# Optimization experiments

Measured on AMD Instinct MI355X. Metric: run time of the kernel, lower is better.

Reference implementation:

```python
import jax, jax.numpy as jnp
import numpy as np

NUM_NODES = 50000
NUM_EDGES = 800000
NUM_FEATURES = 128
HIDDEN = 128
NUM_CLASSES = 40


def setup_inputs() -> dict:
    key = jax.random.key(0)
    ks = jax.random.split(key, 10)
    x = jax.random.normal(ks[0], (NUM_NODES, NUM_FEATURES), dtype=jnp.float32)
    edge_index = jax.random.randint(ks[1], (2, NUM_EDGES), 0, NUM_NODES, dtype=jnp.int32)
    def glorot(k, fan_in, fan_out):
        s = jnp.sqrt(6.0 / (fan_in + fan_out))
        return jax.random.uniform(k, (fan_in, fan_out), jnp.float32, -s, s)
    return {
        "x": x,
        "edge_index": edge_index,
        "W1": glorot(ks[2], NUM_FEATURES, HIDDEN), "b1": jnp.zeros((HIDDEN,), jnp.float32),
        "W2": glorot(ks[3], HIDDEN, HIDDEN),       "b2": jnp.zeros((HIDDEN,), jnp.float32),
        "W3": glorot(ks[4], HIDDEN, HIDDEN),       "b3": jnp.zeros((HIDDEN,), jnp.float32),
        "Wc": glorot(ks[5], HIDDEN, NUM_CLASSES),  "bc": jnp.zeros((NUM_CLASSES,), jnp.float32),
    }


def _gcn_norm(edge_index, num_nodes, dtype):
    # add self-loops, symmetric normalization D^{-1/2} (A+I) D^{-1/2}
    loops = jnp.arange(num_nodes, dtype=edge_index.dtype)
    src = jnp.concatenate([edge_index[0], loops])
    dst = jnp.concatenate([edge_index[1], loops])
    deg = jax.ops.segment_sum(jnp.ones_like(dst, dtype=dtype), dst, num_segments=num_nodes)
    dinv = jnp.where(deg > 0, jax.lax.rsqrt(deg), 0.0)
    norm = dinv[src] * dinv[dst]  # [E + N]
    return src, dst, norm


def _gcn_conv(h, W, b, src, dst, norm, num_nodes):
    h = h @ W                                  # [N, out]
    msg = h[src] * norm[:, None]               # gather + scale  [E+N, out]
    agg = jax.ops.segment_sum(msg, dst, num_segments=num_nodes)
    return agg + b


def reference(x, edge_index, W1, b1, W2, b2, W3, b3, Wc, bc):
    N = x.shape[0]
    src, dst, norm = _gcn_norm(edge_index, N, x.dtype)
    h = jax.nn.relu(_gcn_conv(x, W1, b1, src, dst, norm, N))
    h = jax.nn.relu(_gcn_conv(h, W2, b2, src, dst, norm, N))
    h = jax.nn.relu(_gcn_conv(h, W3, b3, src, dst, norm, N))
    out = h @ Wc + bc
    return (out, h)
```

## Files before the change

kernel.cpp:

```cpp
#include <hip/hip_runtime.h>

typedef float f32x4 __attribute__((ext_vector_type(4)));
typedef short s16x8 __attribute__((ext_vector_type(8)));

__device__ __forceinline__ float us2f(unsigned short u) {
    union { unsigned int i; float f; } v;
    v.i = ((unsigned int)u) << 16;
    return v.f;
}
__device__ __forceinline__ unsigned short f2us(float f) {
    union { unsigned int i; float f; } v; v.f = f;
    unsigned int r = v.i + 0x7fff + ((v.i >> 16) & 1);
    return (unsigned short)(r >> 16);
}

__global__ void k_wprep(const float* __restrict__ W1, const float* __restrict__ W2,
                        const float* __restrict__ W3, const float* __restrict__ Wc,
                        unsigned short* __restrict__ img, int* __restrict__ bcnt) {
    int b = blockIdx.x >> 7;
    int n = threadIdx.x;
    if (b >= 4) { bcnt[n] = 0; bcnt[n + 128] = 0; return; }
    int k = blockIdx.x & 127;
    unsigned short *H, *L;
    float f;
    if (b < 3) {
        const float* W = (b == 0) ? W1 : ((b == 1) ? W2 : W3);
        H = img + b * 32768; L = H + 16384;
        f = W[k * 128 + n];
    } else {
        if (n >= 48) return;
        H = img + 3 * 32768; L = H + 6144;
        f = (n < 40) ? Wc[k * 40 + n] : 0.f;
    }
    unsigned short h = f2us(f);
    unsigned short l = f2us(f - us2f(h));
    int idx = n * 128 + ((((k >> 3) ^ (n & 15))) << 3) + (k & 7);
    H[idx] = h; L[idx] = l;
}

__global__ __launch_bounds__(256) void k_hist(const int* __restrict__ dst, int E, int chunk,
                                              int* __restrict__ bcnt) {
    __shared__ int cnt[256];
    int t = threadIdx.x;
    cnt[t] = 0; __syncthreads();
    int s = blockIdx.x * chunk;
    int e = s + chunk; if (e > E) e = E;
    for (int i = s + t; i < e; i += 256) atomicAdd(&cnt[dst[i] >> 8], 1);
    __syncthreads();
    if (cnt[t]) atomicAdd(&bcnt[t], cnt[t]);
}

__global__ void k_bscan(const int* __restrict__ bcnt, int* __restrict__ bofs,
                        int* __restrict__ gcur) {
    __shared__ int s[256];
    int t = threadIdx.x;
    int v = bcnt[t];
    s[t] = v; __syncthreads();
    for (int off = 1; off < 256; off <<= 1) {
        int x = (t >= off) ? s[t - off] : 0;
        __syncthreads();
        s[t] += x;
        __syncthreads();
    }
    int ex = s[t] - v;
    bofs[t] = ex; gcur[t] = ex;
    if (t == 255) bofs[256] = s[255];
}

__global__ __launch_bounds__(256) void k_scatter1(const int* __restrict__ src,
                                                  const int* __restrict__ dst, int E, int chunk,
                                                  int* __restrict__ gcur,
                                                  unsigned int* __restrict__ pk) {
    __shared__ int cnt[256];
    int t = threadIdx.x;
    cnt[t] = 0; __syncthreads();
    int s = blockIdx.x * chunk;
    int e = s + chunk; if (e > E) e = E;
    for (int i = s + t; i < e; i += 256) atomicAdd(&cnt[dst[i] >> 8], 1);
    __syncthreads();
    int base = atomicAdd(&gcur[t], cnt[t]);
    cnt[t] = base;
    __syncthreads();
    for (int i = s + t; i < e; i += 256) {
        int d = dst[i];
        int slot = atomicAdd(&cnt[d >> 8], 1);
        pk[slot] = ((unsigned int)src[i] << 8) | (unsigned int)(d & 255);
    }
}

__global__ __launch_bounds__(256) void k_degscan(const unsigned int* __restrict__ pk,
                                                 const int* __restrict__ bofs,
                                                 int* __restrict__ row_ptr,
                                                 int* __restrict__ bsum,
                                                 float* __restrict__ dinv, int N) {
    __shared__ int cnt[256];
    __shared__ int s[256];
    int t = threadIdx.x, b = blockIdx.x;
    cnt[t] = 0; __syncthreads();
    int s0 = bofs[b], s1 = bofs[b + 1];
    for (int i = s0 + t; i < s1; i += 256) atomicAdd(&cnt[pk[i] & 255], 1);
    __syncthreads();
    int v = cnt[t];
    s[t] = v; __syncthreads();
    for (int off = 1; off < 256; off <<= 1) {
        int x = (t >= off) ? s[t - off] : 0;
        __syncthreads();
        s[t] += x;
        __syncthreads();
    }
    int node = (b << 8) + t;
    if (node < N) {
        row_ptr[node] = s[t] - v;
        dinv[node] = rsqrtf((float)(v + 1));
    }
    if (t == 255) bsum[b] = s[255];
}

__global__ void k_scan2(int* __restrict__ bsum, int nb) {
    __shared__ int s[256];
    int t = threadIdx.x;
    int v = (t < nb) ? bsum[t] : 0;
    s[t] = v; __syncthreads();
    for (int off = 1; off < 256; off <<= 1) {
        int x = (t >= off) ? s[t - off] : 0;
        __syncthreads();
        s[t] += x;
        __syncthreads();
    }
    if (t < nb) bsum[t] = s[t] - v;
}

__global__ __launch_bounds__(256) void k_scatter2(const unsigned int* __restrict__ pk,
                                                  const int* __restrict__ bofs,
                                                  int* __restrict__ row_ptr,
                                                  const int* __restrict__ bsum,
                                                  int* __restrict__ csr, int N, int E) {
    __shared__ int cur[256];
    int t = threadIdx.x, b = blockIdx.x;
    int node = (b << 8) + t;
    int rp = 0;
    if (node < N) {
        rp = row_ptr[node] + bsum[b];
        row_ptr[node] = rp;
    }
    cur[t] = rp;
    __syncthreads();
    int s = bofs[b], e = bofs[b + 1];
    for (int i = s + t; i < e; i += 256) {
        unsigned int v = pk[i];
        int slot = atomicAdd(&cur[v & 255], 1);
        csr[slot] = (int)(v >> 8);
    }
    if (node == N - 1) row_ptr[N] = E;
}

__global__ __launch_bounds__(256) void k_gemm128m(const float* __restrict__ A,
                                                  const unsigned short* __restrict__ img,
                                                  const float* __restrict__ dinv,
                                                  unsigned short* __restrict__ M, int N) {
    __shared__ __align__(16) unsigned short WsH[16384];
    __shared__ __align__(16) unsigned short WsL[16384];
    int t = threadIdx.x;
    {
        const uint4* s = (const uint4*)img;
        uint4* dH = (uint4*)WsH; uint4* dL = (uint4*)WsL;
#pragma unroll
        for (int i = 0; i < 8; i++) dH[t + i * 256] = s[t + i * 256];
#pragma unroll
        for (int i = 0; i < 8; i++) dL[t + i * 256] = s[2048 + t + i * 256];
    }
    __syncthreads();

    int w = t >> 6, lane = t & 63;
    int m = lane & 15, q = lane >> 4;
    int row0 = blockIdx.x * 64 + w * 16;
    int gr = row0 + m;
    int grc = (gr < N) ? gr : (N - 1);
    const float4* Arow = (const float4*)(A + (size_t)grc * 128);
    int nbase = m * 128;

    f32x4 acc[8];
#pragma unroll
    for (int cb = 0; cb < 8; cb++) { acc[cb][0]=0.f; acc[cb][1]=0.f; acc[cb][2]=0.f; acc[cb][3]=0.f; }

#pragma unroll
    for (int ks = 0; ks < 4; ks++) {
        float4 f0 = Arow[ks * 8 + q * 2];
        float4 f1 = Arow[ks * 8 + q * 2 + 1];
        float fv[8] = {f0.x, f0.y, f0.z, f0.w, f1.x, f1.y, f1.z, f1.w};
        union { unsigned short u[8]; s16x8 v; } ah, al;
#pragma unroll
        for (int j = 0; j < 8; j++) {
            unsigned short h = f2us(fv[j]);
            ah.u[j] = h;
            al.u[j] = f2us(fv[j] - us2f(h));
        }
        int koff = (((ks * 4 + q) ^ m) & 15) << 3;
#pragma unroll
        for (int cb = 0; cb < 8; cb++) {
            int o = cb * 2048 + nbase + koff;
            s16x8 wh = *(const s16x8*)&WsH[o];
            s16x8 wl = *(const s16x8*)&WsL[o];
            acc[cb] = __builtin_amdgcn_mfma_f32_16x16x32_bf16(ah.v, wh, acc[cb], 0, 0, 0);
            acc[cb] = __builtin_amdgcn_mfma_f32_16x16x32_bf16(ah.v, wl, acc[cb], 0, 0, 0);
            acc[cb] = __builtin_amdgcn_mfma_f32_16x16x32_bf16(al.v, wh, acc[cb], 0, 0, 0);
        }
    }

#pragma unroll
    for (int r = 0; r < 4; r++) {
        int grow = row0 + q * 4 + r;
        if (grow < N) {
            float dv = dinv[grow];
#pragma unroll
            for (int cb = 0; cb < 8; cb++)
                M[(size_t)grow * 128 + cb * 16 + m] = f2us(acc[cb][r] * dv);
        }
    }
}

__global__ __launch_bounds__(256) void k_gemm40m(const float* __restrict__ A,
                                                 const unsigned short* __restrict__ img,
                                                 const float* __restrict__ bc,
                                                 float* __restrict__ out, int N) {
    __shared__ __align__(16) unsigned short WsH[6144];
    __shared__ __align__(16) unsigned short WsL[6144];
    int t = threadIdx.x;
    {
        const uint4* s = (const uint4*)img;
        uint4* dH = (uint4*)WsH; uint4* dL = (uint4*)WsL;
#pragma unroll
        for (int i = 0; i < 3; i++) dH[t + i * 256] = s[t + i * 256];
#pragma unroll
        for (int i = 0; i < 3; i++) dL[t + i * 256] = s[768 + t + i * 256];
    }
    __syncthreads();

    int w = t >> 6, lane = t & 63;
    int m = lane & 15, q = lane >> 4;
    int row0 = blockIdx.x * 64 + w * 16;
    int gr = row0 + m;
    int grc = (gr < N) ? gr : (N - 1);
    const float4* Arow = (const float4*)(A + (size_t)grc * 128);
    int nbase = m * 128;

    f32x4 acc[3];
#pragma unroll
    for (int cb = 0; cb < 3; cb++) { acc[cb][0]=0.f; acc[cb][1]=0.f; acc[cb][2]=0.f; acc[cb][3]=0.f; }

#pragma unroll
    for (int ks = 0; ks < 4; ks++) {
        float4 f0 = Arow[ks * 8 + q * 2];
        float4 f1 = Arow[ks * 8 + q * 2 + 1];
        float fv[8] = {f0.x, f0.y, f0.z, f0.w, f1.x, f1.y, f1.z, f1.w};
        union { unsigned short u[8]; s16x8 v; } ah, al;
#pragma unroll
        for (int j = 0; j < 8; j++) {
            unsigned short h = f2us(fv[j]);
            ah.u[j] = h;
            al.u[j] = f2us(fv[j] - us2f(h));
        }
        int koff = (((ks * 4 + q) ^ m) & 15) << 3;
#pragma unroll
        for (int cb = 0; cb < 3; cb++) {
            int o = cb * 2048 + nbase + koff;
            s16x8 wh = *(const s16x8*)&WsH[o];
            s16x8 wl = *(const s16x8*)&WsL[o];
            acc[cb] = __builtin_amdgcn_mfma_f32_16x16x32_bf16(ah.v, wh, acc[cb], 0, 0, 0);
            acc[cb] = __builtin_amdgcn_mfma_f32_16x16x32_bf16(ah.v, wl, acc[cb], 0, 0, 0);
            acc[cb] = __builtin_amdgcn_mfma_f32_16x16x32_bf16(al.v, wh, acc[cb], 0, 0, 0);
        }
    }

#pragma unroll
    for (int r = 0; r < 4; r++) {
        int grow = row0 + q * 4 + r;
        if (grow < N) {
#pragma unroll
            for (int cb = 0; cb < 3; cb++) {
                int col = cb * 16 + m;
                if (col < 40) out[(size_t)grow * 40 + col] = acc[cb][r] + bc[col];
            }
        }
    }
}

__global__ __launch_bounds__(256) void k_gather(const unsigned short* __restrict__ M,
                                                const int* __restrict__ csr,
                                                const int* __restrict__ row_ptr,
                                                const float* __restrict__ dinv,
                                                const float* __restrict__ bias,
                                                float* __restrict__ H, int N) {
    int w    = (blockIdx.x << 2) + (threadIdx.x >> 6);
    int lane = threadIdx.x & 63;
    if (w >= N) return;
    int g  = lane >> 4;
    int sl = lane & 15;

    const uint4* M16 = (const uint4*)M;
    float acc[8];
#pragma unroll
    for (int i = 0; i < 8; i++) acc[i] = 0.f;

    auto accum = [&](uint4 tv) {
        unsigned int uu[4] = {tv.x, tv.y, tv.z, tv.w};
#pragma unroll
        for (int i = 0; i < 4; i++) {
            acc[2 * i]     += us2f((unsigned short)(uu[i] & 0xffffu));
            acc[2 * i + 1] += us2f((unsigned short)(uu[i] >> 16));
        }
    };

    if (g == 0) accum(M16[(size_t)w * 16 + sl]);

    int s0 = row_ptr[w], s1 = row_ptr[w + 1];
    for (int base = s0; base < s1; base += 64) {
        int n = s1 - base; if (n > 64) n = 64;
        int idx = (lane < n) ? csr[base + lane] : 0;
        int full = n >> 2;
        int rem  = n & 3;
        int j = 0;
        for (; j + 4 <= full; j += 4) {
            int u0 = __shfl(idx, (j + 0) * 4 + g);
            int u1 = __shfl(idx, (j + 1) * 4 + g);
            int u2 = __shfl(idx, (j + 2) * 4 + g);
            int u3 = __shfl(idx, (j + 3) * 4 + g);
            uint4 t0 = M16[(size_t)u0 * 16 + sl];
            uint4 t1 = M16[(size_t)u1 * 16 + sl];
            uint4 t2 = M16[(size_t)u2 * 16 + sl];
            uint4 t3 = M16[(size_t)u3 * 16 + sl];
            accum(t0); accum(t1); accum(t2); accum(t3);
        }
        for (; j < full; j++) {
            int u = __shfl(idx, j * 4 + g);
            accum(M16[(size_t)u * 16 + sl]);
        }
        int ur = __shfl(idx, ((full << 2) + g) & 63);
        if (g < rem) accum(M16[(size_t)ur * 16 + sl]);
    }

#pragma unroll
    for (int i = 0; i < 8; i++) {
        acc[i] += __shfl_xor(acc[i], 16);
        acc[i] += __shfl_xor(acc[i], 32);
    }

    float dv = dinv[w];
    const float4* b4 = (const float4*)bias;
    float4 b0 = b4[sl * 2], b1 = b4[sl * 2 + 1];
    float4 o0, o1;
    o0.x = fmaxf(fmaf(dv, acc[0], b0.x), 0.f);
    o0.y = fmaxf(fmaf(dv, acc[1], b0.y), 0.f);
    o0.z = fmaxf(fmaf(dv, acc[2], b0.z), 0.f);
    o0.w = fmaxf(fmaf(dv, acc[3], b0.w), 0.f);
    o1.x = fmaxf(fmaf(dv, acc[4], b1.x), 0.f);
    o1.y = fmaxf(fmaf(dv, acc[5], b1.y), 0.f);
    o1.z = fmaxf(fmaf(dv, acc[6], b1.z), 0.f);
    o1.w = fmaxf(fmaf(dv, acc[7], b1.w), 0.f);

    if (g == 0) {
        float4* H4 = (float4*)H;
        H4[(size_t)w * 32 + sl * 2]     = o0;
        H4[(size_t)w * 32 + sl * 2 + 1] = o1;
    }
}

extern "C" void kernel_launch(void* const* d_in, const int* in_sizes, int n_in,
                              void* d_out, int out_size, void* d_ws, size_t ws_size,
                              hipStream_t stream) {
    const float* x  = (const float*)d_in[0];
    const int*   ei = (const int*)d_in[1];
    const float* W1 = (const float*)d_in[2];
    const float* b1 = (const float*)d_in[3];
    const float* W2 = (const float*)d_in[4];
    const float* b2 = (const float*)d_in[5];
    const float* W3 = (const float*)d_in[6];
    const float* b3 = (const float*)d_in[7];
    const float* Wc = (const float*)d_in[8];
    const float* bc = (const float*)d_in[9];

    const int N = in_sizes[0] / 128;
    const int E = in_sizes[1] / 2;
    const int* src = ei;
    const int* dst = ei + E;

    char* ws = (char*)d_ws;
    size_t off = 0;
    auto alloc = [&](size_t bytes) -> void* {
        void* p = ws + off;
        off = (off + bytes + 255) & ~(size_t)255;
        return p;
    };
    unsigned short* Mbuf = (unsigned short*)alloc((size_t)N * 128 * 2);
    unsigned int* pk     = (unsigned int*)alloc((size_t)E * 4);
    unsigned short* img  = (unsigned short*)alloc((3 * 32768 + 2 * 6144) * 2);
    float* dinv    = (float*)alloc((size_t)N * 4);
    int*   row_ptr = (int*)alloc((size_t)(N + 1) * 4);
    int*   csr     = (int*)alloc((size_t)E * 4);
    int*   bcnt    = (int*)alloc(256 * 4);
    int*   bofs    = (int*)alloc(257 * 4);
    int*   gcur    = (int*)alloc(256 * 4);
    int*   bsum    = (int*)alloc(256 * 4);

    float* out  = (float*)d_out;
    float* hbuf = out + (size_t)N * 40;

    const int nb  = (N + 255) / 256;
    const int NB  = (N + 255) >> 8;
    const int G1  = 256;
    const int chunk = (E + G1 - 1) / G1;

    k_wprep<<<513, 128, 0, stream>>>(W1, W2, W3, Wc, img, bcnt);

    k_hist<<<G1, 256, 0, stream>>>(dst, E, chunk, bcnt);
    k_bscan<<<1, 256, 0, stream>>>(bcnt, bofs, gcur);
    k_scatter1<<<G1, 256, 0, stream>>>(src, dst, E, chunk, gcur, pk);
    k_degscan<<<NB, 256, 0, stream>>>(pk, bofs, row_ptr, bsum, dinv, N);
    k_scan2<<<1, 256, 0, stream>>>(bsum, nb);
    k_scatter2<<<NB, 256, 0, stream>>>(pk, bofs, row_ptr, bsum, csr, N, E);

    const int gb  = (N + 63) / 64;
    const int gab = (N + 3) / 4;

    k_gemm128m<<<gb, 256, 0, stream>>>(x, img, dinv, Mbuf, N);
    k_gather<<<gab, 256, 0, stream>>>(Mbuf, csr, row_ptr, dinv, b1, hbuf, N);
    k_gemm128m<<<gb, 256, 0, stream>>>(hbuf, img + 32768, dinv, Mbuf, N);
    k_gather<<<gab, 256, 0, stream>>>(Mbuf, csr, row_ptr, dinv, b2, hbuf, N);
    k_gemm128m<<<gb, 256, 0, stream>>>(hbuf, img + 2 * 32768, dinv, Mbuf, N);
    k_gather<<<gab, 256, 0, stream>>>(Mbuf, csr, row_ptr, dinv, b3, hbuf, N);
    k_gemm40m<<<gb, 256, 0, stream>>>(hbuf, img + 3 * 32768, bc, out, N);
}
```

Baseline: 285.1 us.

## Split gather into feature quarters and store intermediate activations as bf16

The message buffer is laid out as four feature-quarter planes. The gather kernel now runs a 4-way grid in y, one quarter per block row, so each quarter plane (about 3.2 MB) can stay cache-resident during the random neighbour gathers. Layers 1 and 2 write bf16 activations with nontemporal stores, and the next GEMM reads them directly as bf16, which drops the split hi/lo conversion and one MFMA per step. In exchange, the edge lists are walked four times, and the hidden activations lose precision by being rounded to bf16.

```diff
diff --git a/kernel.cpp b/kernel.cpp
--- a/kernel.cpp
+++ b/kernel.cpp
@@ -154,7 +154,8 @@
     if (node == N - 1) row_ptr[N] = E;
 }
 
-__global__ __launch_bounds__(256) void k_gemm128m(const float* __restrict__ A,
+template <bool ABF16>
+__global__ __launch_bounds__(256) void k_gemm128m(const void* __restrict__ Ap,
                                                   const unsigned short* __restrict__ img,
                                                   const float* __restrict__ dinv,
                                                   unsigned short* __restrict__ M, int N) {
@@ -168,6 +169,79 @@
         for (int i = 0; i < 8; i++) dH[t + i * 256] = s[t + i * 256];
 #pragma unroll
         for (int i = 0; i < 8; i++) dL[t + i * 256] = s[2048 + t + i * 256];
+    }
+    __syncthreads();
+
+    int w = t >> 6, lane = t & 63;
+    int m = lane & 15, q = lane >> 4;
+    int row0 = blockIdx.x * 64 + w * 16;
+    int gr = row0 + m;
+    int grc = (gr < N) ? gr : (N - 1);
+    const float* A32 = (const float*)Ap + (size_t)grc * 128;
+    const unsigned short* A16 = (const unsigned short*)Ap + (size_t)grc * 128;
+    int nbase = m * 128;
+
+    f32x4 acc[8];
+#pragma unroll
+    for (int cb = 0; cb < 8; cb++) { acc[cb][0]=0.f; acc[cb][1]=0.f; acc[cb][2]=0.f; acc[cb][3]=0.f; }
+
+#pragma unroll
+    for (int ks = 0; ks < 4; ks++) {
+        union { unsigned short u[8]; s16x8 v; } ah, al;
+        if constexpr (ABF16) {
+            ah.v = *(const s16x8*)&A16[ks * 32 + q * 8];
+        } else {
+            float4 f0 = ((const float4*)A32)[ks * 8 + q * 2];
+            float4 f1 = ((const float4*)A32)[ks * 8 + q * 2 + 1];
+            float fv[8] = {f0.x, f0.y, f0.z, f0.w, f1.x, f1.y, f1.z, f1.w};
+#pragma unroll
+            for (int j = 0; j < 8; j++) {
+                unsigned short h = f2us(fv[j]);
+                ah.u[j] = h;
+                al.u[j] = f2us(fv[j] - us2f(h));
+            }
+        }
+        int koff = (((ks * 4 + q) ^ m) & 15) << 3;
+#pragma unroll
+        for (int cb = 0; cb < 8; cb++) {
+            int o = cb * 2048 + nbase + koff;
+            s16x8 wh = *(const s16x8*)&WsH[o];
+            s16x8 wl = *(const s16x8*)&WsL[o];
+            acc[cb] = __builtin_amdgcn_mfma_f32_16x16x32_bf16(ah.v, wh, acc[cb], 0, 0, 0);
+            acc[cb] = __builtin_amdgcn_mfma_f32_16x16x32_bf16(ah.v, wl, acc[cb], 0, 0, 0);
+            if constexpr (!ABF16)
+                acc[cb] = __builtin_amdgcn_mfma_f32_16x16x32_bf16(al.v, wh, acc[cb], 0, 0, 0);
+        }
+    }
+
+#pragma unroll
+    for (int r = 0; r < 4; r++) {
+        int grow = row0 + q * 4 + r;
+        if (grow < N) {
+            float dv = dinv[grow];
+#pragma unroll
+            for (int cb = 0; cb < 8; cb++) {
+                M[((size_t)(cb >> 1) * N + grow) * 32 + (cb & 1) * 16 + m] =
+                    f2us(acc[cb][r] * dv);
+            }
+        }
+    }
+}
+
+__global__ __launch_bounds__(256) void k_gemm40m(const float* __restrict__ A,
+                                                 const unsigned short* __restrict__ img,
+                                                 const float* __restrict__ bc,
+                                                 float* __restrict__ out, int N) {
+    __shared__ __align__(16) unsigned short WsH[6144];
+    __shared__ __align__(16) unsigned short WsL[6144];
+    int t = threadIdx.x;
+    {
+        const uint4* s = (const uint4*)img;
+        uint4* dH = (uint4*)WsH; uint4* dL = (uint4*)WsL;
+#pragma unroll
+        for (int i = 0; i < 3; i++) dH[t + i * 256] = s[t + i * 256];
+#pragma unroll
+        for (int i = 0; i < 3; i++) dL[t + i * 256] = s[768 + t + i * 256];
     }
     __syncthreads();
 
@@ -179,71 +253,6 @@
     const float4* Arow = (const float4*)(A + (size_t)grc * 128);
     int nbase = m * 128;
 
-    f32x4 acc[8];
-#pragma unroll
-    for (int cb = 0; cb < 8; cb++) { acc[cb][0]=0.f; acc[cb][1]=0.f; acc[cb][2]=0.f; acc[cb][3]=0.f; }
-
-#pragma unroll
-    for (int ks = 0; ks < 4; ks++) {
-        float4 f0 = Arow[ks * 8 + q * 2];
-        float4 f1 = Arow[ks * 8 + q * 2 + 1];
-        float fv[8] = {f0.x, f0.y, f0.z, f0.w, f1.x, f1.y, f1.z, f1.w};
-        union { unsigned short u[8]; s16x8 v; } ah, al;
-#pragma unroll
-        for (int j = 0; j < 8; j++) {
-            unsigned short h = f2us(fv[j]);
-            ah.u[j] = h;
-            al.u[j] = f2us(fv[j] - us2f(h));
-        }
-        int koff = (((ks * 4 + q) ^ m) & 15) << 3;
-#pragma unroll
-        for (int cb = 0; cb < 8; cb++) {
-            int o = cb * 2048 + nbase + koff;
-            s16x8 wh = *(const s16x8*)&WsH[o];
-            s16x8 wl = *(const s16x8*)&WsL[o];
-            acc[cb] = __builtin_amdgcn_mfma_f32_16x16x32_bf16(ah.v, wh, acc[cb], 0, 0, 0);
-            acc[cb] = __builtin_amdgcn_mfma_f32_16x16x32_bf16(ah.v, wl, acc[cb], 0, 0, 0);
-            acc[cb] = __builtin_amdgcn_mfma_f32_16x16x32_bf16(al.v, wh, acc[cb], 0, 0, 0);
-        }
-    }
-
-#pragma unroll
-    for (int r = 0; r < 4; r++) {
-        int grow = row0 + q * 4 + r;
-        if (grow < N) {
-            float dv = dinv[grow];
-#pragma unroll
-            for (int cb = 0; cb < 8; cb++)
-                M[(size_t)grow * 128 + cb * 16 + m] = f2us(acc[cb][r] * dv);
-        }
-    }
-}
-
-__global__ __launch_bounds__(256) void k_gemm40m(const float* __restrict__ A,
-                                                 const unsigned short* __restrict__ img,
-                                                 const float* __restrict__ bc,
-                                                 float* __restrict__ out, int N) {
-    __shared__ __align__(16) unsigned short WsH[6144];
-    __shared__ __align__(16) unsigned short WsL[6144];
-    int t = threadIdx.x;
-    {
-        const uint4* s = (const uint4*)img;
-        uint4* dH = (uint4*)WsH; uint4* dL = (uint4*)WsL;
-#pragma unroll
-        for (int i = 0; i < 3; i++) dH[t + i * 256] = s[t + i * 256];
-#pragma unroll
-        for (int i = 0; i < 3; i++) dL[t + i * 256] = s[768 + t + i * 256];
-    }
-    __syncthreads();
-
-    int w = t >> 6, lane = t & 63;
-    int m = lane & 15, q = lane >> 4;
-    int row0 = blockIdx.x * 64 + w * 16;
-    int gr = row0 + m;
-    int grc = (gr < N) ? gr : (N - 1);
-    const float4* Arow = (const float4*)(A + (size_t)grc * 128);
-    int nbase = m * 128;
-
     f32x4 acc[3];
 #pragma unroll
     for (int cb = 0; cb < 3; cb++) { acc[cb][0]=0.f; acc[cb][1]=0.f; acc[cb][2]=0.f; acc[cb][3]=0.f; }
@@ -285,33 +294,28 @@
     }
 }
 
+template <bool OUT_BF16>
 __global__ __launch_bounds__(256) void k_gather(const unsigned short* __restrict__ M,
                                                 const int* __restrict__ csr,
                                                 const int* __restrict__ row_ptr,
                                                 const float* __restrict__ dinv,
                                                 const float* __restrict__ bias,
-                                                float* __restrict__ H, int N) {
+                                                void* __restrict__ H, int N) {
+    int qtr  = blockIdx.y;
     int w    = (blockIdx.x << 2) + (threadIdx.x >> 6);
     int lane = threadIdx.x & 63;
     if (w >= N) return;
     int g  = lane >> 4;
     int sl = lane & 15;
 
-    const uint4* M16 = (const uint4*)M;
-    float acc[8];
-#pragma unroll
-    for (int i = 0; i < 8; i++) acc[i] = 0.f;
-
-    auto accum = [&](uint4 tv) {
-        unsigned int uu[4] = {tv.x, tv.y, tv.z, tv.w};
-#pragma unroll
-        for (int i = 0; i < 4; i++) {
-            acc[2 * i]     += us2f((unsigned short)(uu[i] & 0xffffu));
-            acc[2 * i + 1] += us2f((unsigned short)(uu[i] >> 16));
-        }
+    const unsigned int* Mq = (const unsigned int*)M + (size_t)qtr * N * 16;
+    float ax = 0.f, ay = 0.f;
+    auto accum = [&](unsigned int v) {
+        ax += us2f((unsigned short)(v & 0xffffu));
+        ay += us2f((unsigned short)(v >> 16));
     };
 
-    if (g == 0) accum(M16[(size_t)w * 16 + sl]);
+    if (g == 0) accum(Mq[(size_t)w * 16 + sl]);
 
     int s0 = row_ptr[w], s1 = row_ptr[w + 1];
     for (int base = s0; base < s1; base += 64) {
@@ -325,43 +329,36 @@
             int u1 = __shfl(idx, (j + 1) * 4 + g);
             int u2 = __shfl(idx, (j + 2) * 4 + g);
             int u3 = __shfl(idx, (j + 3) * 4 + g);
-            uint4 t0 = M16[(size_t)u0 * 16 + sl];
-            uint4 t1 = M16[(size_t)u1 * 16 + sl];
-            uint4 t2 = M16[(size_t)u2 * 16 + sl];
-            uint4 t3 = M16[(size_t)u3 * 16 + sl];
+            unsigned int t0 = Mq[(size_t)u0 * 16 + sl];
+            unsigned int t1 = Mq[(size_t)u1 * 16 + sl];
+            unsigned int t2 = Mq[(size_t)u2 * 16 + sl];
+            unsigned int t3 = Mq[(size_t)u3 * 16 + sl];
             accum(t0); accum(t1); accum(t2); accum(t3);
         }
         for (; j < full; j++) {
             int u = __shfl(idx, j * 4 + g);
-            accum(M16[(size_t)u * 16 + sl]);
+            accum(Mq[(size_t)u * 16 + sl]);
         }
         int ur = __shfl(idx, ((full << 2) + g) & 63);
-        if (g < rem) accum(M16[(size_t)ur * 16 + sl]);
-    }
-
-#pragma unroll
-    for (int i = 0; i < 8; i++) {
-        acc[i] += __shfl_xor(acc[i], 16);
-        acc[i] += __shfl_xor(acc[i], 32);
-    }
-
-    float dv = dinv[w];
-    const float4* b4 = (const float4*)bias;
-    float4 b0 = b4[sl * 2], b1 = b4[sl * 2 + 1];
-    float4 o0, o1;
-    o0.x = fmaxf(fmaf(dv, acc[0], b0.x), 0.f);
-    o0.y = fmaxf(fmaf(dv, acc[1], b0.y), 0.f);
-    o0.z = fmaxf(fmaf(dv, acc[2], b0.z), 0.f);
-    o0.w = fmaxf(fmaf(dv, acc[3], b0.w), 0.f);
-    o1.x = fmaxf(fmaf(dv, acc[4], b1.x), 0.f);
-    o1.y = fmaxf(fmaf(dv, acc[5], b1.y), 0.f);
-    o1.z = fmaxf(fmaf(dv, acc[6], b1.z), 0.f);
-    o1.w = fmaxf(fmaf(dv, acc[7], b1.w), 0.f);
+        if (g < rem) accum(Mq[(size_t)ur * 16 + sl]);
+    }
+
+    ax += __shfl_xor(ax, 16); ax += __shfl_xor(ax, 32);
+    ay += __shfl_xor(ay, 16); ay += __shfl_xor(ay, 32);
 
     if (g == 0) {
-        float4* H4 = (float4*)H;
-        H4[(size_t)w * 32 + sl * 2]     = o0;
-        H4[(size_t)w * 32 + sl * 2 + 1] = o1;
+        float dv = dinv[w];
+        int f0 = qtr * 32 + sl * 2;
+        float ox = fmaxf(fmaf(dv, ax, bias[f0]), 0.f);
+        float oy = fmaxf(fmaf(dv, ay, bias[f0 + 1]), 0.f);
+        if constexpr (OUT_BF16) {
+            unsigned int pkd = (unsigned int)f2us(ox) | ((unsigned int)f2us(oy) << 16);
+            __builtin_nontemporal_store(pkd,
+                (unsigned int*)H + (size_t)w * 64 + qtr * 16 + sl);
+        } else {
+            float* Hp = (float*)H + (size_t)w * 128 + f0;
+            Hp[0] = ox; Hp[1] = oy;
+        }
     }
 }
 
@@ -392,6 +389,7 @@
         return p;
     };
     unsigned short* Mbuf = (unsigned short*)alloc((size_t)N * 128 * 2);
+    unsigned short* Hb   = (unsigned short*)alloc((size_t)N * 128 * 2);
     unsigned int* pk     = (unsigned int*)alloc((size_t)E * 4);
     unsigned short* img  = (unsigned short*)alloc((3 * 32768 + 2 * 6144) * 2);
     float* dinv    = (float*)alloc((size_t)N * 4);
@@ -420,13 +418,13 @@
     k_scatter2<<<NB, 256, 0, stream>>>(pk, bofs, row_ptr, bsum, csr, N, E);
 
     const int gb  = (N + 63) / 64;
-    const int gab = (N + 3) / 4;
-
-    k_gemm128m<<<gb, 256, 0, stream>>>(x, img, dinv, Mbuf, N);
-    k_gather<<<gab, 256, 0, stream>>>(Mbuf, csr, row_ptr, dinv, b1, hbuf, N);
-    k_gemm128m<<<gb, 256, 0, stream>>>(hbuf, img + 32768, dinv, Mbuf, N);
-    k_gather<<<gab, 256, 0, stream>>>(Mbuf, csr, row_ptr, dinv, b2, hbuf, N);
-    k_gemm128m<<<gb, 256, 0, stream>>>(hbuf, img + 2 * 32768, dinv, Mbuf, N);
-    k_gather<<<gab, 256, 0, stream>>>(Mbuf, csr, row_ptr, dinv, b3, hbuf, N);
+    const dim3 gg((N + 3) / 4, 4, 1);
+
+    k_gemm128m<false><<<gb, 256, 0, stream>>>(x, img, dinv, Mbuf, N);
+    k_gather<true><<<gg, 256, 0, stream>>>(Mbuf, csr, row_ptr, dinv, b1, Hb, N);
+    k_gemm128m<true><<<gb, 256, 0, stream>>>(Hb, img + 32768, dinv, Mbuf, N);
+    k_gather<true><<<gg, 256, 0, stream>>>(Mbuf, csr, row_ptr, dinv, b2, Hb, N);
+    k_gemm128m<true><<<gb, 256, 0, stream>>>(Hb, img + 2 * 32768, dinv, Mbuf, N);
+    k_gather<false><<<gg, 256, 0, stream>>>(Mbuf, csr, row_ptr, dinv, b3, hbuf, N);
     k_gemm40m<<<gb, 256, 0, stream>>>(hbuf, img + 3 * 32768, bc, out, N);
 }
```

Result: slower. 407.6 us (+43.0%).
